# Performance work log

Hardware: AMD Instinct MI355X
Metric: run time of the kernel (lower is better)

Reference implementation:

```python
import jax, jax.numpy as jnp
import numpy as np
from jax import lax

VOCAB, EMB, H, L_CTX = 5, 64, 256, 100
HG = 2 * H  # generator hidden = 512


def lstm_cell(x, h, c, Wih, Whh, b):
    # PyTorch gate order: i, f, g, o
    z = x @ Wih.T + h @ Whh.T + b
    i, f, g, o = jnp.split(z, 4, axis=-1)
    c = jax.nn.sigmoid(f) * c + jax.nn.sigmoid(i) * jnp.tanh(g)
    h = jax.nn.sigmoid(o) * jnp.tanh(c)
    return h, c


def run_lstm(xs, Wih, Whh, b, hidden):
    # xs: [T, B, D] -> ys: [T, B, hidden]
    B = xs.shape[1]
    h0 = jnp.zeros((B, hidden), xs.dtype)

    def step(carry, x):
        h, c = carry
        h, c = lstm_cell(x, h, c, Wih, Whh, b)
        return (h, c), h

    _, ys = lax.scan(step, (h0, h0), xs)
    return ys


def bidir_layer(xs, Wih, Whh, b):
    # Wih/Whh/b stacked over directions: [2, ...]
    yf = run_lstm(xs, Wih[0], Whh[0], b[0], H)
    yb = run_lstm(xs[::-1], Wih[1], Whh[1], b[1], H)[::-1]
    return jnp.concatenate([yf, yb], axis=-1)  # [T, B, 2H]


def setup_inputs() -> dict:
    key = jax.random.key(0)
    ks = iter(jax.random.split(key, 24))
    s = 1.0 / np.sqrt(H)  # pytorch-style uniform scale -> use normal*s

    def w(shape):
        return (jax.random.normal(next(ks), shape, jnp.float32) * s).astype(jnp.float32)

    B = 1024
    inp = {
        "left_context": jax.random.randint(next(ks), (B, L_CTX), 0, VOCAB),
        "right_context": jax.random.randint(next(ks), (B, L_CTX), 0, VOCAB),
        "target_length": 256,
        "emb": w((VOCAB, EMB)),
        # bidirectional context LSTM, layer 0 (in=64) and layer 1 (in=512)
        "ctx0_Wih": w((2, 4 * H, EMB)),
        "ctx0_Whh": w((2, 4 * H, H)),
        "ctx0_b": w((2, 4 * H)),
        "ctx1_Wih": w((2, 4 * H, 2 * H)),
        "ctx1_Whh": w((2, 4 * H, H)),
        "ctx1_b": w((2, 4 * H)),
        # generator LSTM (hidden=512), layer 0 (in=64) and layer 1 (in=512)
        "gen0_Wih": w((4 * HG, EMB)),
        "gen0_Whh": w((4 * HG, HG)),
        "gen0_b": w((4 * HG,)),
        "gen1_Wih": w((4 * HG, HG)),
        "gen1_Whh": w((4 * HG, HG)),
        "gen1_b": w((4 * HG,)),
        "out_W": w((VOCAB, HG)),
        "out_b": w((VOCAB,)),
    }
    return inp


def reference(left_context, right_context, target_length, emb,
              ctx0_Wih, ctx0_Whh, ctx0_b, ctx1_Wih, ctx1_Whh, ctx1_b,
              gen0_Wih, gen0_Whh, gen0_b, gen1_Wih, gen1_Whh, gen1_b,
              out_W, out_b):
    B = left_context.shape[0]

    def encode(tokens):
        x = emb[tokens].transpose(1, 0, 2)          # [L, B, 64]
        x = bidir_layer(x, ctx0_Wih, ctx0_Whh, ctx0_b)  # dropout: eval -> identity
        x = bidir_layer(x, ctx1_Wih, ctx1_Whh, ctx1_b)
        return x                                     # [L, B, 512]

    left_final = encode(left_context)[-1]            # [B, 512]
    right_final = encode(right_context)[0]           # [B, 512]
    combined = (left_final + right_final) * 0.5

    # h_0 = combined repeated over both generator layers; c_0 = 0
    zeros = jnp.zeros((B, HG), combined.dtype)
    tok0 = jnp.zeros((B,), jnp.int32)

    def dec_step(carry, _):
        h0, c0, h1, c1, tok = carry
        x = emb[tok]                                 # [B, 64]
        h0, c0 = lstm_cell(x, h0, c0, gen0_Wih, gen0_Whh, gen0_b)
        h1, c1 = lstm_cell(h0, h1, c1, gen1_Wih, gen1_Whh, gen1_b)
        logits = h1 @ out_W.T + out_b                # dropout: eval -> identity
        tok = jnp.argmax(logits, axis=-1)
        return (h0, c0, h1, c1, tok), logits

    _, logits = lax.scan(dec_step, (combined, zeros, combined, zeros, tok0),
                         None, length=target_length)
    return logits.transpose(1, 0, 2)                 # [B, T, vocab]
```

## Files before the change

### kernel.cpp

```cpp
#include <hip/hip_runtime.h>


#define L_SEQ 100
#define BATCH 1024
#define HCTX 256
#define HG 512
#define TDEC 256

typedef __attribute__((ext_vector_type(8))) short bf16x8;
typedef __attribute__((ext_vector_type(4))) float f32x4;

__device__ __forceinline__ float sigf(float x){ return 1.0f/(1.0f+expf(-x)); }
__device__ __forceinline__ unsigned short f2bf(float x){
  unsigned int u = __float_as_uint(x);
  return (unsigned short)((u + 0x7fffu + ((u>>16)&1u)) >> 16);
}
__device__ __forceinline__ float bf2f(unsigned short h){
  return __uint_as_float(((unsigned int)h)<<16);
}

__global__ void pack_w(const float* __restrict__ W, int G, int K, int KTtot, int kt0,
                       unsigned short* __restrict__ hi, unsigned short* __restrict__ lo){
  int idx = blockIdx.x*blockDim.x + threadIdx.x;
  int kt_n = K/32;
  int total = (G/16)*kt_n*64;
  if (idx >= total) return;
  int lane = idx & 63;
  int ktl = (idx>>6) % kt_n;
  int gt  = (idx>>6) / kt_n;
  int g = gt*16 + (lane & 15);
  int k = ktl*32 + (lane>>4)*8;
  const float* src = W + (size_t)g*K + k;
  size_t dst = (((size_t)gt*KTtot + (kt0 + ktl))*64 + lane)*8;
  #pragma unroll
  for (int j=0;j<8;j++){
    float x = src[j];
    unsigned short h = f2bf(x);
    hi[dst+j] = h;
    lo[dst+j] = f2bf(x - bf2f(h));
  }
}

__global__ void embprep(const float* __restrict__ emb,
                        const float* __restrict__ c0Wih, const float* __restrict__ c0b,
                        const float* __restrict__ g0Wih, const float* __restrict__ g0b,
                        float* __restrict__ ectx0, float* __restrict__ egen0){
  int idx = blockIdx.x*blockDim.x + threadIdx.x;
  if (idx < 2*5*1024){
    int d = idx / 5120;
    int v = (idx / 1024) % 5;
    int j = idx % 1024;
    const float* w = c0Wih + ((size_t)d*1024 + j)*64;
    const float* e = emb + v*64;
    float s = c0b[d*1024 + j];
    #pragma unroll
    for (int k=0;k<64;k++) s += e[k]*w[k];
    ectx0[idx] = s;
  } else if (idx < 2*5*1024 + 5*2048){
    int i2 = idx - 10240;
    int v = i2 / 2048;
    int j = i2 % 2048;
    const float* w = g0Wih + (size_t)j*64;
    const float* e = emb + v*64;
    float s = g0b[j];
    #pragma unroll
    for (int k=0;k<64;k++) s += e[k]*w[k];
    egen0[i2] = s;
  }
}

__global__ void __launch_bounds__(512,1) ctx_l0_mfma(
    const int* __restrict__ toks,
    const float* __restrict__ ectx0,
    const unsigned short* __restrict__ wh, const unsigned short* __restrict__ wl,
    unsigned short* __restrict__ y0h, unsigned short* __restrict__ y0l)
{
  const int id  = blockIdx.x;
  const int dir = (id >> 2) & 1;
  const int bx  = ((id >> 3) << 2) | (id & 3);
  const int e0  = bx * 16;
  const int lane = threadIdx.x & 63;
  const int w    = threadIdx.x >> 6;
  const int lo16 = lane & 15, kgrp = lane >> 4;

  __shared__ unsigned short hsh[16*256];
  __shared__ unsigned short hsl[16*256];
  __shared__ float cs[16*256];
  for (int i=threadIdx.x;i<16*256;i+=512){ hsh[i]=0; hsl[i]=0; cs[i]=0.f; }
  __syncthreads();

  const unsigned short* pbh[4][2];
  const unsigned short* pbl[4][2];
  #pragma unroll
  for (int g=0;g<4;g++){
    #pragma unroll
    for (int st=0;st<2;st++){
      int ct = g*16 + w*2 + st;
      size_t off = (size_t)dir*1024*256 + ((size_t)(ct*8)*64 + lane)*8;
      pbh[g][st] = wh + off; pbl[g][st] = wl + off;
    }
  }
  const unsigned aoff0 = (unsigned)(lo16*512 + kgrp*16);
  const unsigned axor  = ((unsigned)(lo16 & 7)) << 4;

  for (int s=0;s<L_SEQ;s++){
    const int t = dir ? (L_SEQ-1-s) : s;
    f32x4 zero = {0.f,0.f,0.f,0.f};
    f32x4 acc[4][2];
    #pragma unroll
    for (int g=0;g<4;g++){
      #pragma unroll
      for (int st=0;st<2;st++) acc[g][st] = zero;
    }
    #pragma unroll 2
    for (int kt=0;kt<8;kt++){
      unsigned ao = (aoff0 + kt*64) ^ axor;
      bf16x8 ah = *(const bf16x8*)((const char*)hsh + ao);
      bf16x8 al = *(const bf16x8*)((const char*)hsl + ao);
      #pragma unroll
      for (int g=0;g<4;g++){
        #pragma unroll
        for (int st=0;st<2;st++){
          bf16x8 bh = *(const bf16x8*)(pbh[g][st] + (size_t)kt*512);
          bf16x8 bl = *(const bf16x8*)(pbl[g][st] + (size_t)kt*512);
          acc[g][st] = __builtin_amdgcn_mfma_f32_16x16x32_bf16(ah,bh,acc[g][st],0,0,0);
          acc[g][st] = __builtin_amdgcn_mfma_f32_16x16x32_bf16(al,bh,acc[g][st],0,0,0);
          acc[g][st] = __builtin_amdgcn_mfma_f32_16x16x32_bf16(ah,bl,acc[g][st],0,0,0);
        }
      }
    }
    __syncthreads();
    int tkr[4];
    #pragma unroll
    for (int r=0;r<4;r++) tkr[r] = toks[(e0 + kgrp*4 + r)*L_SEQ + t];
    #pragma unroll
    for (int st=0;st<2;st++){
      const int unit = w*32 + st*16 + lo16;
      #pragma unroll
      for (int r=0;r<4;r++){
        const int row = kgrp*4 + r;
        const int e = e0 + row;
        const float* ep = ectx0 + ((size_t)(dir*5 + tkr[r]))*1024 + unit;
        float zi = acc[0][st][r] + ep[0];
        float zf = acc[1][st][r] + ep[256];
        float zg = acc[2][st][r] + ep[512];
        float zo = acc[3][st][r] + ep[768];
        int ci = row*256 + unit;
        float c = sigf(zf)*cs[ci] + sigf(zi)*tanhf(zg);
        float h = sigf(zo)*tanhf(c);
        cs[ci] = c;
        unsigned short hb = f2bf(h), lb = f2bf(h - bf2f(hb));
        unsigned hoff = ((unsigned)(row*512 + unit*2)) ^ (((unsigned)(row & 7)) << 4);
        *(unsigned short*)((char*)hsh + hoff) = hb;
        *(unsigned short*)((char*)hsl + hoff) = lb;
        size_t yo = ((size_t)t*BATCH + e)*512 + dir*256 + unit;
        y0h[yo] = hb; y0l[yo] = lb;
      }
    }
    __syncthreads();
  }
}

__global__ void __launch_bounds__(512,1) ctx_l1_mfma(
    const unsigned short* __restrict__ y0h, const unsigned short* __restrict__ y0l,
    const unsigned short* __restrict__ wh, const unsigned short* __restrict__ wl,
    const float* __restrict__ bias,
    float* __restrict__ finals, int t_store)
{
  const int id  = blockIdx.x;
  const int dir = (id >> 2) & 1;
  const int bx  = ((id >> 3) << 2) | (id & 3);
  const int e0  = bx * 16;
  const int lane = threadIdx.x & 63;
  const int w    = threadIdx.x >> 6;
  const int lo16 = lane & 15, kgrp = lane >> 4;

  __shared__ unsigned short xsh[16*512];
  __shared__ unsigned short xsl[16*512];
  __shared__ unsigned short hsh[16*256];
  __shared__ unsigned short hsl[16*256];
  __shared__ float cs[16*256];
  for (int i=threadIdx.x;i<16*256;i+=512){ hsh[i]=0; hsl[i]=0; cs[i]=0.f; }

  float bb[4][2];
  #pragma unroll
  for (int g=0;g<4;g++){
    #pragma unroll
    for (int st=0;st<2;st++)
      bb[g][st] = bias[dir*1024 + g*256 + w*32 + st*16 + lo16];
  }
  const unsigned short* pbh[4][2];
  const unsigned short* pbl[4][2];
  #pragma unroll
  for (int g=0;g<4;g++){
    #pragma unroll
    for (int st=0;st<2;st++){
      int ct = g*16 + w*2 + st;
      size_t off = (size_t)dir*1024*768 + ((size_t)(ct*24)*64 + lane)*8;
      pbh[g][st] = wh + off; pbl[g][st] = wl + off;
    }
  }
  const unsigned axor = ((unsigned)(lo16 & 7)) << 4;
  __syncthreads();

  for (int s=0;s<L_SEQ;s++){
    const int t = dir ? (L_SEQ-1-s) : s;
    #pragma unroll
    for (int cc=0; cc<2; cc++){
      int ci = threadIdx.x + cc*512;
      int row = ci >> 6, cr = ci & 63;
      const unsigned short* srcbase = y0h + ((size_t)t*BATCH + e0 + row)*512 + cr*8;
      const unsigned short* srcbasel = y0l + ((size_t)t*BATCH + e0 + row)*512 + cr*8;
      uint4 vh = *(const uint4*)srcbase;
      uint4 vl = *(const uint4*)srcbasel;
      unsigned xo = ((unsigned)(row*1024 + cr*16)) ^ (((unsigned)(row & 7)) << 4);
      *(uint4*)((char*)xsh + xo) = vh;
      *(uint4*)((char*)xsl + xo) = vl;
    }
    __syncthreads();
    f32x4 zero = {0.f,0.f,0.f,0.f};
    f32x4 acc[4][2];
    #pragma unroll
    for (int g=0;g<4;g++){
      #pragma unroll
      for (int st=0;st<2;st++) acc[g][st] = zero;
    }
    #pragma unroll 2
    for (int kt=0;kt<16;kt++){
      unsigned ao = ((unsigned)(lo16*1024 + kt*64 + kgrp*16)) ^ axor;
      bf16x8 ah = *(const bf16x8*)((const char*)xsh + ao);
      bf16x8 al = *(const bf16x8*)((const char*)xsl + ao);
      #pragma unroll
      for (int g=0;g<4;g++){
        #pragma unroll
        for (int st=0;st<2;st++){
          bf16x8 bh = *(const bf16x8*)(pbh[g][st] + (size_t)kt*512);
          bf16x8 bl = *(const bf16x8*)(pbl[g][st] + (size_t)kt*512);
          acc[g][st] = __builtin_amdgcn_mfma_f32_16x16x32_bf16(ah,bh,acc[g][st],0,0,0);
          acc[g][st] = __builtin_amdgcn_mfma_f32_16x16x32_bf16(al,bh,acc[g][st],0,0,0);
          acc[g][st] = __builtin_amdgcn_mfma_f32_16x16x32_bf16(ah,bl,acc[g][st],0,0,0);
        }
      }
    }
    #pragma unroll 2
    for (int kt=16;kt<24;kt++){
      unsigned ao = ((unsigned)(lo16*512 + (kt-16)*64 + kgrp*16)) ^ axor;
      bf16x8 ah = *(const bf16x8*)((const char*)hsh + ao);
      bf16x8 al = *(const bf16x8*)((const char*)hsl + ao);
      #pragma unroll
      for (int g=0;g<4;g++){
        #pragma unroll
        for (int st=0;st<2;st++){
          bf16x8 bh = *(const bf16x8*)(pbh[g][st] + (size_t)kt*512);
          bf16x8 bl = *(const bf16x8*)(pbl[g][st] + (size_t)kt*512);
          acc[g][st] = __builtin_amdgcn_mfma_f32_16x16x32_bf16(ah,bh,acc[g][st],0,0,0);
          acc[g][st] = __builtin_amdgcn_mfma_f32_16x16x32_bf16(al,bh,acc[g][st],0,0,0);
          acc[g][st] = __builtin_amdgcn_mfma_f32_16x16x32_bf16(ah,bl,acc[g][st],0,0,0);
        }
      }
    }
    __syncthreads();
    #pragma unroll
    for (int st=0;st<2;st++){
      const int unit = w*32 + st*16 + lo16;
      #pragma unroll
      for (int r=0;r<4;r++){
        const int row = kgrp*4 + r;
        float zi = acc[0][st][r] + bb[0][st];
        float zf = acc[1][st][r] + bb[1][st];
        float zg = acc[2][st][r] + bb[2][st];
        float zo = acc[3][st][r] + bb[3][st];
        int ci = row*256 + unit;
        float c = sigf(zf)*cs[ci] + sigf(zi)*tanhf(zg);
        float h = sigf(zo)*tanhf(c);
        cs[ci] = c;
        unsigned short hb = f2bf(h), lb = f2bf(h - bf2f(hb));
        unsigned hoff = ((unsigned)(row*512 + unit*2)) ^ (((unsigned)(row & 7)) << 4);
        *(unsigned short*)((char*)hsh + hoff) = hb;
        *(unsigned short*)((char*)hsl + hoff) = lb;
        if (t == t_store)
          finals[(size_t)(e0 + row)*512 + dir*256 + unit] = h;
      }
    }
    __syncthreads();
  }
}

__global__ void combine_init2(const float* __restrict__ lf, const float* __restrict__ rf,
                              unsigned short* __restrict__ h0h, unsigned short* __restrict__ h0l,
                              unsigned short* __restrict__ h1h, unsigned short* __restrict__ h1l,
                              float* __restrict__ c0, float* __restrict__ c1,
                              int* __restrict__ tok){
  int i = blockIdx.x*blockDim.x + threadIdx.x;
  if (i < BATCH*HG){
    float v = 0.5f*(lf[i]+rf[i]);
    unsigned short h = f2bf(v);
    unsigned short l = f2bf(v - bf2f(h));
    h0h[i]=h; h0l[i]=l; h1h[i]=h; h1l[i]=l;
    c0[i]=0.f; c1[i]=0.f;
  }
  if (i < BATCH) tok[i]=0;
}

__global__ void __launch_bounds__(512,2) dec_l0_mfma(
    const int* __restrict__ tok,
    const float* __restrict__ egen0,
    const unsigned short* __restrict__ wh, const unsigned short* __restrict__ wl,
    const unsigned short* __restrict__ hih, const unsigned short* __restrict__ hil,
    unsigned short* __restrict__ hoh, unsigned short* __restrict__ hol,
    float* __restrict__ cst)
{
  const int bid = blockIdx.x;
  const int by = bid & 15;
  const int bx = bid >> 4;
  const int e0 = bx * 64;
  const int lane = threadIdx.x & 63;
  const int w = threadIdx.x >> 6;
  const int wm = w & 3;
  const int wu = w >> 2;
  const int ut = by*2 + wu;
  const int lo16 = lane & 15;
  const int kgrp = lane >> 4;
  const int row = e0 + wm*16 + lo16;

  const unsigned short* pah = hih + (size_t)row*512 + kgrp*8;
  const unsigned short* pal = hil + (size_t)row*512 + kgrp*8;
  const unsigned short* pb[8];
  #pragma unroll
  for (int q=0;q<4;q++){
    size_t off = ((size_t)(q*32+ut)*16*64 + lane)*8;
    pb[q]   = wh + off;
    pb[q+4] = wl + off;
  }
  f32x4 zero = {0.f,0.f,0.f,0.f};
  f32x4 acc[4] = {zero, zero, zero, zero};
  #pragma unroll 2
  for (int ks=0; ks<16; ks++){
    bf16x8 ah = *(const bf16x8*)(pah + ks*32);
    bf16x8 al = *(const bf16x8*)(pal + ks*32);
    #pragma unroll
    for (int q=0;q<4;q++){
      bf16x8 bh = *(const bf16x8*)(pb[q]   + ks*512);
      bf16x8 bl = *(const bf16x8*)(pb[q+4] + ks*512);
      acc[q] = __builtin_amdgcn_mfma_f32_16x16x32_bf16(ah, bh, acc[q], 0,0,0);
      acc[q] = __builtin_amdgcn_mfma_f32_16x16x32_bf16(al, bh, acc[q], 0,0,0);
      acc[q] = __builtin_amdgcn_mfma_f32_16x16x32_bf16(ah, bl, acc[q], 0,0,0);
    }
  }
  const int u = ut*16 + lo16;
  const int r0 = e0 + wm*16 + kgrp*4;
  #pragma unroll
  for (int r=0;r<4;r++){
    const int e = r0 + r;
    const int tk = tok[e];
    const float* ep = egen0 + (size_t)tk*2048 + u;
    float zi = acc[0][r] + ep[0];
    float zf = acc[1][r] + ep[512];
    float zg = acc[2][r] + ep[1024];
    float zo = acc[3][r] + ep[1536];
    const size_t idx = (size_t)e*512 + u;
    float c = sigf(zf)*cst[idx] + sigf(zi)*tanhf(zg);
    float h = sigf(zo)*tanhf(c);
    cst[idx] = c;
    unsigned short hb = f2bf(h);
    hoh[idx] = hb;
    hol[idx] = f2bf(h - bf2f(hb));
  }
}

__global__ void __launch_bounds__(512,2) dec_l1_mfma(
    const unsigned short* __restrict__ xh, const unsigned short* __restrict__ xl,
    const unsigned short* __restrict__ wh, const unsigned short* __restrict__ wl,
    const float* __restrict__ bias,
    const unsigned short* __restrict__ hih, const unsigned short* __restrict__ hil,
    unsigned short* __restrict__ hoh, unsigned short* __restrict__ hol,
    float* __restrict__ cst)
{
  const int bid = blockIdx.x;
  const int by = bid & 15;
  const int bx = bid >> 4;
  const int e0 = bx * 64;
  const int lane = threadIdx.x & 63;
  const int w = threadIdx.x >> 6;
  const int wm = w & 3;
  const int wu = w >> 2;
  const int ut = by*2 + wu;
  const int lo16 = lane & 15;
  const int kgrp = lane >> 4;
  const int row = e0 + wm*16 + lo16;

  const unsigned short* pxh = xh  + (size_t)row*512 + kgrp*8;
  const unsigned short* pxl = xl  + (size_t)row*512 + kgrp*8;
  const unsigned short* pah = hih + (size_t)row*512 + kgrp*8;
  const unsigned short* pal = hil + (size_t)row*512 + kgrp*8;
  const unsigned short* pb[8];
  #pragma unroll
  for (int q=0;q<4;q++){
    size_t off = ((size_t)(q*32+ut)*32*64 + lane)*8;
    pb[q]   = wh + off;
    pb[q+4] = wl + off;
  }
  f32x4 zero = {0.f,0.f,0.f,0.f};
  f32x4 acc[4] = {zero, zero, zero, zero};
  #pragma unroll 2
  for (int ks=0; ks<16; ks++){
    bf16x8 ah = *(const bf16x8*)(pxh + ks*32);
    bf16x8 al = *(const bf16x8*)(pxl + ks*32);
    #pragma unroll
    for (int q=0;q<4;q++){
      bf16x8 bh = *(const bf16x8*)(pb[q]   + ks*512);
      bf16x8 bl = *(const bf16x8*)(pb[q+4] + ks*512);
      acc[q] = __builtin_amdgcn_mfma_f32_16x16x32_bf16(ah, bh, acc[q], 0,0,0);
      acc[q] = __builtin_amdgcn_mfma_f32_16x16x32_bf16(al, bh, acc[q], 0,0,0);
      acc[q] = __builtin_amdgcn_mfma_f32_16x16x32_bf16(ah, bl, acc[q], 0,0,0);
    }
  }
  #pragma unroll 2
  for (int ks=16; ks<32; ks++){
    bf16x8 ah = *(const bf16x8*)(pah + (ks-16)*32);
    bf16x8 al = *(const bf16x8*)(pal + (ks-16)*32);
    #pragma unroll
    for (int q=0;q<4;q++){
      bf16x8 bh = *(const bf16x8*)(pb[q]   + ks*512);
      bf16x8 bl = *(const bf16x8*)(pb[q+4] + ks*512);
      acc[q] = __builtin_amdgcn_mfma_f32_16x16x32_bf16(ah, bh, acc[q], 0,0,0);
      acc[q] = __builtin_amdgcn_mfma_f32_16x16x32_bf16(al, bh, acc[q], 0,0,0);
      acc[q] = __builtin_amdgcn_mfma_f32_16x16x32_bf16(ah, bl, acc[q], 0,0,0);
    }
  }
  const int u = ut*16 + lo16;
  const int r0 = e0 + wm*16 + kgrp*4;
  const float b0 = bias[u], b1 = bias[512+u], b2 = bias[1024+u], b3 = bias[1536+u];
  #pragma unroll
  for (int r=0;r<4;r++){
    const int e = r0 + r;
    float zi = acc[0][r] + b0;
    float zf = acc[1][r] + b1;
    float zg = acc[2][r] + b2;
    float zo = acc[3][r] + b3;
    const size_t idx = (size_t)e*512 + u;
    float c = sigf(zf)*cst[idx] + sigf(zi)*tanhf(zg);
    float h = sigf(zo)*tanhf(c);
    cst[idx] = c;
    unsigned short hb = f2bf(h);
    hoh[idx] = hb;
    hol[idx] = f2bf(h - bf2f(hb));
  }
}

__global__ void dec_out(const unsigned short* __restrict__ h1h,
                        const unsigned short* __restrict__ h1l,
                        const float* __restrict__ outW,
                        const float* __restrict__ outb,
                        float* __restrict__ out,
                        int* __restrict__ tok, int t){
  const int lane = threadIdx.x & 63;
  const int e = blockIdx.x*4 + (threadIdx.x >> 6);
  const unsigned short* hh = h1h + (size_t)e*512;
  const unsigned short* hl = h1l + (size_t)e*512;
  float s0=0,s1=0,s2=0,s3=0,s4=0;
  for (int k=lane;k<512;k+=64){
    float hv = bf2f(hh[k]) + bf2f(hl[k]);
    s0 += hv*outW[k];
    s1 += hv*outW[512+k];
    s2 += hv*outW[1024+k];
    s3 += hv*outW[1536+k];
    s4 += hv*outW[2048+k];
  }
  #pragma unroll
  for (int off=32; off>0; off>>=1){
    s0 += __shfl_down(s0, off);
    s1 += __shfl_down(s1, off);
    s2 += __shfl_down(s2, off);
    s3 += __shfl_down(s3, off);
    s4 += __shfl_down(s4, off);
  }
  if (lane==0){
    float l[5] = { s0+outb[0], s1+outb[1], s2+outb[2], s3+outb[3], s4+outb[4] };
    float* op = out + ((size_t)e*TDEC + t)*5;
    float best = l[0]; int bi = 0;
    op[0] = l[0];
    #pragma unroll
    for (int v=1;v<5;v++){
      op[v] = l[v];
      if (l[v] > best){ best = l[v]; bi = v; }
    }
    tok[e] = bi;
  }
}

extern "C" void kernel_launch(void* const* d_in, const int* in_sizes, int n_in,
                              void* d_out, int out_size, void* d_ws, size_t ws_size,
                              hipStream_t stream){
  (void)in_sizes; (void)n_in; (void)out_size;
  const int*   leftc    = (const int*)d_in[0];
  const int*   rightc   = (const int*)d_in[1];
  const float* emb      = (const float*)d_in[3];
  const float* ctx0_Wih = (const float*)d_in[4];
  const float* ctx0_Whh = (const float*)d_in[5];
  const float* ctx0_b   = (const float*)d_in[6];
  const float* ctx1_Wih = (const float*)d_in[7];
  const float* ctx1_Whh = (const float*)d_in[8];
  const float* ctx1_b   = (const float*)d_in[9];
  const float* gen0_Wih = (const float*)d_in[10];
  const float* gen0_Whh = (const float*)d_in[11];
  const float* gen0_b   = (const float*)d_in[12];
  const float* gen1_Wih = (const float*)d_in[13];
  const float* gen1_Whh = (const float*)d_in[14];
  const float* gen1_b   = (const float*)d_in[15];
  const float* out_W    = (const float*)d_in[16];
  const float* out_b    = (const float*)d_in[17];
  float* out = (float*)d_out;

  char* p = (char*)d_ws;
  auto carve = [&](size_t nfloats)->float*{
    float* r = (float*)p;
    p += ((nfloats*sizeof(float) + 255) & ~(size_t)255);
    return r;
  };
  auto carveu = [&](size_t nush)->unsigned short*{
    return (unsigned short*)carve((nush + 1)/2);
  };
  float* ectx0  = carve(2*5*1024);
  float* egen0  = carve(5*2048);
  float* leftF  = carve((size_t)BATCH*HG);
  float* rightF = carve((size_t)BATCH*HG);
  float* c0s    = carve((size_t)BATCH*HG);
  float* c1s    = carve((size_t)BATCH*HG);
  unsigned short* c0pkh = carveu((size_t)2*1024*256);
  unsigned short* c0pkl = carveu((size_t)2*1024*256);
  unsigned short* c1pkh = carveu((size_t)2*1024*768);
  unsigned short* c1pkl = carveu((size_t)2*1024*768);
  unsigned short* pk0h = carveu((size_t)2048*512);
  unsigned short* pk0l = carveu((size_t)2048*512);
  unsigned short* pk1h = carveu((size_t)2048*1024);
  unsigned short* pk1l = carveu((size_t)2048*1024);
  unsigned short* h0ha = carveu((size_t)BATCH*HG);
  unsigned short* h0la = carveu((size_t)BATCH*HG);
  unsigned short* h0hb = carveu((size_t)BATCH*HG);
  unsigned short* h0lb = carveu((size_t)BATCH*HG);
  unsigned short* h1ha = carveu((size_t)BATCH*HG);
  unsigned short* h1la = carveu((size_t)BATCH*HG);
  unsigned short* h1hb = carveu((size_t)BATCH*HG);
  unsigned short* h1lb = carveu((size_t)BATCH*HG);
  int*   tok    = (int*)carve(BATCH);
  unsigned short* y0h = carveu((size_t)L_SEQ*BATCH*512);
  unsigned short* y0l = carveu((size_t)L_SEQ*BATCH*512);
  if ((size_t)(p - (char*)d_ws) > ws_size) return;

  for (int d=0; d<2; d++){
    pack_w<<<128, 256, 0, stream>>>(ctx0_Whh + (size_t)d*1024*256, 1024, 256, 8, 0,
                                    c0pkh + (size_t)d*1024*256/ (size_t)1 * 0 + (size_t)d*262144,
                                    c0pkl + (size_t)d*262144);
    pack_w<<<256, 256, 0, stream>>>(ctx1_Wih + (size_t)d*1024*512, 1024, 512, 24, 0,
                                    c1pkh + (size_t)d*786432, c1pkl + (size_t)d*786432);
    pack_w<<<128, 256, 0, stream>>>(ctx1_Whh + (size_t)d*1024*256, 1024, 256, 24, 16,
                                    c1pkh + (size_t)d*786432, c1pkl + (size_t)d*786432);
  }
  pack_w<<<512, 256, 0, stream>>>(gen0_Whh, 2048, 512, 16,  0, pk0h, pk0l);
  pack_w<<<512, 256, 0, stream>>>(gen1_Wih, 2048, 512, 32,  0, pk1h, pk1l);
  pack_w<<<512, 256, 0, stream>>>(gen1_Whh, 2048, 512, 32, 16, pk1h, pk1l);

  embprep<<<(20480+255)/256, 256, 0, stream>>>(emb, ctx0_Wih, ctx0_b,
                                               gen0_Wih, gen0_b, ectx0, egen0);

  ctx_l0_mfma<<<128, 512, 0, stream>>>(leftc, ectx0, c0pkh, c0pkl, y0h, y0l);
  ctx_l1_mfma<<<128, 512, 0, stream>>>(y0h, y0l, c1pkh, c1pkl, ctx1_b, leftF, L_SEQ-1);
  ctx_l0_mfma<<<128, 512, 0, stream>>>(rightc, ectx0, c0pkh, c0pkl, y0h, y0l);
  ctx_l1_mfma<<<128, 512, 0, stream>>>(y0h, y0l, c1pkh, c1pkl, ctx1_b, rightF, 0);

  combine_init2<<<(BATCH*HG+255)/256, 256, 0, stream>>>(leftF, rightF,
                                                        h0ha, h0la, h1ha, h1la,
                                                        c0s, c1s, tok);

  for (int t=0;t<TDEC;t++){
    unsigned short* h0ih = (t&1)? h0hb : h0ha;
    unsigned short* h0il = (t&1)? h0lb : h0la;
    unsigned short* h0oh = (t&1)? h0ha : h0hb;
    unsigned short* h0ol = (t&1)? h0la : h0lb;
    unsigned short* h1ih = (t&1)? h1hb : h1ha;
    unsigned short* h1il = (t&1)? h1lb : h1la;
    unsigned short* h1oh = (t&1)? h1ha : h1hb;
    unsigned short* h1ol = (t&1)? h1la : h1lb;
    dec_l0_mfma<<<256, 512, 0, stream>>>(tok, egen0, pk0h, pk0l,
                                         h0ih, h0il, h0oh, h0ol, c0s);
    dec_l1_mfma<<<256, 512, 0, stream>>>(h0oh, h0ol, pk1h, pk1l, gen1_b,
                                         h1ih, h1il, h1oh, h1ol, c1s);
    dec_out<<<256, 256, 0, stream>>>(h1oh, h1ol, out_W, out_b, out, tok, t);
  }
}
```

Baseline: 23.13 ms.

## Fuse decoder timesteps into one persistent cooperative kernel with grid syncs

Replaces the 768 per-timestep launches of the two generator LSTM layers and the output projection with a single cooperative kernel that loops over time. Layers are separated by grid.sync, and the cell states stay in registers instead of global memory. The output projection is fused as a shuffle reduction plus atomicAdd into a bias-prefilled output, and the next token is recomputed from the previous logits. The MFMA accumulators are also split into three separate chains. The cost is two grid-wide barriers per step, a dependence on all 256 blocks being co-resident, and atomics whose summation order is not fixed.

```diff
diff --git a/kernel.cpp b/kernel.cpp
--- a/kernel.cpp
+++ b/kernel.cpp
@@ -1,4 +1,7 @@
 #include <hip/hip_runtime.h>
+#include <hip/hip_cooperative_groups.h>
+
+namespace cg = cooperative_groups;
 
 
 #define L_SEQ 100
@@ -69,6 +72,11 @@
   }
 }
 
+__global__ void prefill_out(float* __restrict__ out, const float* __restrict__ outb){
+  int i = blockIdx.x*blockDim.x + threadIdx.x;
+  if (i < BATCH*TDEC*5) out[i] = outb[i%5];
+}
+
 __global__ void __launch_bounds__(512,1) ctx_l0_mfma(
     const int* __restrict__ toks,
     const float* __restrict__ ectx0,
@@ -288,28 +296,29 @@
 
 __global__ void combine_init2(const float* __restrict__ lf, const float* __restrict__ rf,
                               unsigned short* __restrict__ h0h, unsigned short* __restrict__ h0l,
-                              unsigned short* __restrict__ h1h, unsigned short* __restrict__ h1l,
-                              float* __restrict__ c0, float* __restrict__ c1,
-                              int* __restrict__ tok){
+                              unsigned short* __restrict__ h1h, unsigned short* __restrict__ h1l){
   int i = blockIdx.x*blockDim.x + threadIdx.x;
   if (i < BATCH*HG){
     float v = 0.5f*(lf[i]+rf[i]);
     unsigned short h = f2bf(v);
     unsigned short l = f2bf(v - bf2f(h));
     h0h[i]=h; h0l[i]=l; h1h[i]=h; h1l[i]=l;
-    c0[i]=0.f; c1[i]=0.f;
-  }
-  if (i < BATCH) tok[i]=0;
-}
-
-__global__ void __launch_bounds__(512,2) dec_l0_mfma(
-    const int* __restrict__ tok,
+  }
+}
+
+__global__ void __launch_bounds__(512,2) dec_persist(
     const float* __restrict__ egen0,
-    const unsigned short* __restrict__ wh, const unsigned short* __restrict__ wl,
-    const unsigned short* __restrict__ hih, const unsigned short* __restrict__ hil,
-    unsigned short* __restrict__ hoh, unsigned short* __restrict__ hol,
-    float* __restrict__ cst)
+    const unsigned short* __restrict__ w0h, const unsigned short* __restrict__ w0l,
+    const unsigned short* __restrict__ w1h, const unsigned short* __restrict__ w1l,
+    const float* __restrict__ bias1,
+    const float* __restrict__ outW,
+    unsigned short* __restrict__ h0ha, unsigned short* __restrict__ h0la,
+    unsigned short* __restrict__ h0hb, unsigned short* __restrict__ h0lb,
+    unsigned short* __restrict__ h1ha, unsigned short* __restrict__ h1la,
+    unsigned short* __restrict__ h1hb, unsigned short* __restrict__ h1lb,
+    float* __restrict__ out)
 {
+  cg::grid_group grid = cg::this_grid();
   const int bid = blockIdx.x;
   const int by = bid & 15;
   const int bx = bid >> 4;
@@ -321,171 +330,154 @@
   const int ut = by*2 + wu;
   const int lo16 = lane & 15;
   const int kgrp = lane >> 4;
-  const int row = e0 + wm*16 + lo16;
-
-  const unsigned short* pah = hih + (size_t)row*512 + kgrp*8;
-  const unsigned short* pal = hil + (size_t)row*512 + kgrp*8;
-  const unsigned short* pb[8];
+  const int arow = e0 + wm*16 + lo16;
+  const int u = ut*16 + lo16;
+  const int r0 = e0 + wm*16 + kgrp*4;
+
+  const float b10 = bias1[u], b11 = bias1[512+u];
+  const float b12 = bias1[1024+u], b13 = bias1[1536+u];
+  float ow[5];
+  #pragma unroll
+  for (int v=0;v<5;v++) ow[v] = outW[v*512 + u];
+
+  const unsigned short* p0[8];
+  const unsigned short* p1[8];
   #pragma unroll
   for (int q=0;q<4;q++){
-    size_t off = ((size_t)(q*32+ut)*16*64 + lane)*8;
-    pb[q]   = wh + off;
-    pb[q+4] = wl + off;
-  }
-  f32x4 zero = {0.f,0.f,0.f,0.f};
-  f32x4 acc[4] = {zero, zero, zero, zero};
-  #pragma unroll 2
-  for (int ks=0; ks<16; ks++){
-    bf16x8 ah = *(const bf16x8*)(pah + ks*32);
-    bf16x8 al = *(const bf16x8*)(pal + ks*32);
-    #pragma unroll
-    for (int q=0;q<4;q++){
-      bf16x8 bh = *(const bf16x8*)(pb[q]   + ks*512);
-      bf16x8 bl = *(const bf16x8*)(pb[q+4] + ks*512);
-      acc[q] = __builtin_amdgcn_mfma_f32_16x16x32_bf16(ah, bh, acc[q], 0,0,0);
-      acc[q] = __builtin_amdgcn_mfma_f32_16x16x32_bf16(al, bh, acc[q], 0,0,0);
-      acc[q] = __builtin_amdgcn_mfma_f32_16x16x32_bf16(ah, bl, acc[q], 0,0,0);
-    }
-  }
-  const int u = ut*16 + lo16;
-  const int r0 = e0 + wm*16 + kgrp*4;
-  #pragma unroll
-  for (int r=0;r<4;r++){
-    const int e = r0 + r;
-    const int tk = tok[e];
-    const float* ep = egen0 + (size_t)tk*2048 + u;
-    float zi = acc[0][r] + ep[0];
-    float zf = acc[1][r] + ep[512];
-    float zg = acc[2][r] + ep[1024];
-    float zo = acc[3][r] + ep[1536];
-    const size_t idx = (size_t)e*512 + u;
-    float c = sigf(zf)*cst[idx] + sigf(zi)*tanhf(zg);
-    float h = sigf(zo)*tanhf(c);
-    cst[idx] = c;
-    unsigned short hb = f2bf(h);
-    hoh[idx] = hb;
-    hol[idx] = f2bf(h - bf2f(hb));
-  }
-}
-
-__global__ void __launch_bounds__(512,2) dec_l1_mfma(
-    const unsigned short* __restrict__ xh, const unsigned short* __restrict__ xl,
-    const unsigned short* __restrict__ wh, const unsigned short* __restrict__ wl,
-    const float* __restrict__ bias,
-    const unsigned short* __restrict__ hih, const unsigned short* __restrict__ hil,
-    unsigned short* __restrict__ hoh, unsigned short* __restrict__ hol,
-    float* __restrict__ cst)
-{
-  const int bid = blockIdx.x;
-  const int by = bid & 15;
-  const int bx = bid >> 4;
-  const int e0 = bx * 64;
-  const int lane = threadIdx.x & 63;
-  const int w = threadIdx.x >> 6;
-  const int wm = w & 3;
-  const int wu = w >> 2;
-  const int ut = by*2 + wu;
-  const int lo16 = lane & 15;
-  const int kgrp = lane >> 4;
-  const int row = e0 + wm*16 + lo16;
-
-  const unsigned short* pxh = xh  + (size_t)row*512 + kgrp*8;
-  const unsigned short* pxl = xl  + (size_t)row*512 + kgrp*8;
-  const unsigned short* pah = hih + (size_t)row*512 + kgrp*8;
-  const unsigned short* pal = hil + (size_t)row*512 + kgrp*8;
-  const unsigned short* pb[8];
-  #pragma unroll
-  for (int q=0;q<4;q++){
-    size_t off = ((size_t)(q*32+ut)*32*64 + lane)*8;
-    pb[q]   = wh + off;
-    pb[q+4] = wl + off;
-  }
-  f32x4 zero = {0.f,0.f,0.f,0.f};
-  f32x4 acc[4] = {zero, zero, zero, zero};
-  #pragma unroll 2
-  for (int ks=0; ks<16; ks++){
-    bf16x8 ah = *(const bf16x8*)(pxh + ks*32);
-    bf16x8 al = *(const bf16x8*)(pxl + ks*32);
-    #pragma unroll
-    for (int q=0;q<4;q++){
-      bf16x8 bh = *(const bf16x8*)(pb[q]   + ks*512);
-      bf16x8 bl = *(const bf16x8*)(pb[q+4] + ks*512);
-      acc[q] = __builtin_amdgcn_mfma_f32_16x16x32_bf16(ah, bh, acc[q], 0,0,0);
-      acc[q] = __builtin_amdgcn_mfma_f32_16x16x32_bf16(al, bh, acc[q], 0,0,0);
-      acc[q] = __builtin_amdgcn_mfma_f32_16x16x32_bf16(ah, bl, acc[q], 0,0,0);
-    }
-  }
-  #pragma unroll 2
-  for (int ks=16; ks<32; ks++){
-    bf16x8 ah = *(const bf16x8*)(pah + (ks-16)*32);
-    bf16x8 al = *(const bf16x8*)(pal + (ks-16)*32);
-    #pragma unroll
-    for (int q=0;q<4;q++){
-      bf16x8 bh = *(const bf16x8*)(pb[q]   + ks*512);
-      bf16x8 bl = *(const bf16x8*)(pb[q+4] + ks*512);
-      acc[q] = __builtin_amdgcn_mfma_f32_16x16x32_bf16(ah, bh, acc[q], 0,0,0);
-      acc[q] = __builtin_amdgcn_mfma_f32_16x16x32_bf16(al, bh, acc[q], 0,0,0);
-      acc[q] = __builtin_amdgcn_mfma_f32_16x16x32_bf16(ah, bl, acc[q], 0,0,0);
-    }
-  }
-  const int u = ut*16 + lo16;
-  const int r0 = e0 + wm*16 + kgrp*4;
-  const float b0 = bias[u], b1 = bias[512+u], b2 = bias[1024+u], b3 = bias[1536+u];
-  #pragma unroll
-  for (int r=0;r<4;r++){
-    const int e = r0 + r;
-    float zi = acc[0][r] + b0;
-    float zf = acc[1][r] + b1;
-    float zg = acc[2][r] + b2;
-    float zo = acc[3][r] + b3;
-    const size_t idx = (size_t)e*512 + u;
-    float c = sigf(zf)*cst[idx] + sigf(zi)*tanhf(zg);
-    float h = sigf(zo)*tanhf(c);
-    cst[idx] = c;
-    unsigned short hb = f2bf(h);
-    hoh[idx] = hb;
-    hol[idx] = f2bf(h - bf2f(hb));
-  }
-}
-
-__global__ void dec_out(const unsigned short* __restrict__ h1h,
-                        const unsigned short* __restrict__ h1l,
-                        const float* __restrict__ outW,
-                        const float* __restrict__ outb,
-                        float* __restrict__ out,
-                        int* __restrict__ tok, int t){
-  const int lane = threadIdx.x & 63;
-  const int e = blockIdx.x*4 + (threadIdx.x >> 6);
-  const unsigned short* hh = h1h + (size_t)e*512;
-  const unsigned short* hl = h1l + (size_t)e*512;
-  float s0=0,s1=0,s2=0,s3=0,s4=0;
-  for (int k=lane;k<512;k+=64){
-    float hv = bf2f(hh[k]) + bf2f(hl[k]);
-    s0 += hv*outW[k];
-    s1 += hv*outW[512+k];
-    s2 += hv*outW[1024+k];
-    s3 += hv*outW[1536+k];
-    s4 += hv*outW[2048+k];
-  }
-  #pragma unroll
-  for (int off=32; off>0; off>>=1){
-    s0 += __shfl_down(s0, off);
-    s1 += __shfl_down(s1, off);
-    s2 += __shfl_down(s2, off);
-    s3 += __shfl_down(s3, off);
-    s4 += __shfl_down(s4, off);
-  }
-  if (lane==0){
-    float l[5] = { s0+outb[0], s1+outb[1], s2+outb[2], s3+outb[3], s4+outb[4] };
-    float* op = out + ((size_t)e*TDEC + t)*5;
-    float best = l[0]; int bi = 0;
-    op[0] = l[0];
-    #pragma unroll
-    for (int v=1;v<5;v++){
-      op[v] = l[v];
-      if (l[v] > best){ best = l[v]; bi = v; }
-    }
-    tok[e] = bi;
+    size_t o0 = ((size_t)(q*32+ut)*16*64 + lane)*8;
+    p0[q] = w0h + o0; p0[q+4] = w0l + o0;
+    size_t o1 = ((size_t)(q*32+ut)*32*64 + lane)*8;
+    p1[q] = w1h + o1; p1[q+4] = w1l + o1;
+  }
+  float c0r[4] = {0.f,0.f,0.f,0.f};
+  float c1r[4] = {0.f,0.f,0.f,0.f};
+  const f32x4 z4 = {0.f,0.f,0.f,0.f};
+
+  for (int t=0;t<TDEC;t++){
+    const unsigned short* h0ih = (t&1)? h0hb : h0ha;
+    const unsigned short* h0il = (t&1)? h0lb : h0la;
+    unsigned short* h0oh = (t&1)? h0ha : h0hb;
+    unsigned short* h0ol = (t&1)? h0la : h0lb;
+    const unsigned short* h1ih = (t&1)? h1hb : h1ha;
+    const unsigned short* h1il = (t&1)? h1lb : h1la;
+    unsigned short* h1oh = (t&1)? h1ha : h1hb;
+    unsigned short* h1ol = (t&1)? h1la : h1lb;
+
+    {
+      const unsigned short* pah = h0ih + (size_t)arow*512 + kgrp*8;
+      const unsigned short* pal = h0il + (size_t)arow*512 + kgrp*8;
+      f32x4 aHH[4]={z4,z4,z4,z4}, aLH[4]={z4,z4,z4,z4}, aHL[4]={z4,z4,z4,z4};
+      #pragma unroll 2
+      for (int ks=0;ks<16;ks++){
+        bf16x8 ah = *(const bf16x8*)(pah + ks*32);
+        bf16x8 al = *(const bf16x8*)(pal + ks*32);
+        #pragma unroll
+        for (int q=0;q<4;q++){
+          bf16x8 bh = *(const bf16x8*)(p0[q]   + (size_t)ks*512);
+          bf16x8 bl = *(const bf16x8*)(p0[q+4] + (size_t)ks*512);
+          aHH[q] = __builtin_amdgcn_mfma_f32_16x16x32_bf16(ah,bh,aHH[q],0,0,0);
+          aLH[q] = __builtin_amdgcn_mfma_f32_16x16x32_bf16(al,bh,aLH[q],0,0,0);
+          aHL[q] = __builtin_amdgcn_mfma_f32_16x16x32_bf16(ah,bl,aHL[q],0,0,0);
+        }
+      }
+      int tkr[4];
+      #pragma unroll
+      for (int r=0;r<4;r++){
+        int tk = 0;
+        if (t > 0){
+          const float* lp = out + ((size_t)(r0+r)*TDEC + (t-1))*5;
+          float l0=lp[0],l1=lp[1],l2=lp[2],l3=lp[3],l4=lp[4];
+          float best=l0;
+          if (l1>best){best=l1;tk=1;}
+          if (l2>best){best=l2;tk=2;}
+          if (l3>best){best=l3;tk=3;}
+          if (l4>best){best=l4;tk=4;}
+        }
+        tkr[r]=tk;
+      }
+      #pragma unroll
+      for (int r=0;r<4;r++){
+        const int e = r0 + r;
+        const float* ep = egen0 + (size_t)tkr[r]*2048 + u;
+        float zi = aHH[0][r]+aLH[0][r]+aHL[0][r] + ep[0];
+        float zf = aHH[1][r]+aLH[1][r]+aHL[1][r] + ep[512];
+        float zg = aHH[2][r]+aLH[2][r]+aHL[2][r] + ep[1024];
+        float zo = aHH[3][r]+aLH[3][r]+aHL[3][r] + ep[1536];
+        float c = sigf(zf)*c0r[r] + sigf(zi)*tanhf(zg);
+        float h = sigf(zo)*tanhf(c);
+        c0r[r] = c;
+        const size_t idx = (size_t)e*512 + u;
+        unsigned short hb = f2bf(h);
+        h0oh[idx] = hb;
+        h0ol[idx] = f2bf(h - bf2f(hb));
+      }
+    }
+    grid.sync();
+
+    {
+      const unsigned short* pxh = h0oh + (size_t)arow*512 + kgrp*8;
+      const unsigned short* pxl = h0ol + (size_t)arow*512 + kgrp*8;
+      const unsigned short* pah = h1ih + (size_t)arow*512 + kgrp*8;
+      const unsigned short* pal = h1il + (size_t)arow*512 + kgrp*8;
+      f32x4 aHH[4]={z4,z4,z4,z4}, aLH[4]={z4,z4,z4,z4}, aHL[4]={z4,z4,z4,z4};
+      #pragma unroll 2
+      for (int ks=0;ks<16;ks++){
+        bf16x8 ah = *(const bf16x8*)(pxh + ks*32);
+        bf16x8 al = *(const bf16x8*)(pxl + ks*32);
+        #pragma unroll
+        for (int q=0;q<4;q++){
+          bf16x8 bh = *(const bf16x8*)(p1[q]   + (size_t)ks*512);
+          bf16x8 bl = *(const bf16x8*)(p1[q+4] + (size_t)ks*512);
+          aHH[q] = __builtin_amdgcn_mfma_f32_16x16x32_bf16(ah,bh,aHH[q],0,0,0);
+          aLH[q] = __builtin_amdgcn_mfma_f32_16x16x32_bf16(al,bh,aLH[q],0,0,0);
+          aHL[q] = __builtin_amdgcn_mfma_f32_16x16x32_bf16(ah,bl,aHL[q],0,0,0);
+        }
+      }
+      #pragma unroll 2
+      for (int ks=16;ks<32;ks++){
+        bf16x8 ah = *(const bf16x8*)(pah + (ks-16)*32);
+        bf16x8 al = *(const bf16x8*)(pal + (ks-16)*32);
+        #pragma unroll
+        for (int q=0;q<4;q++){
+          bf16x8 bh = *(const bf16x8*)(p1[q]   + (size_t)ks*512);
+          bf16x8 bl = *(const bf16x8*)(p1[q+4] + (size_t)ks*512);
+          aHH[q] = __builtin_amdgcn_mfma_f32_16x16x32_bf16(ah,bh,aHH[q],0,0,0);
+          aLH[q] = __builtin_amdgcn_mfma_f32_16x16x32_bf16(al,bh,aLH[q],0,0,0);
+          aHL[q] = __builtin_amdgcn_mfma_f32_16x16x32_bf16(ah,bl,aHL[q],0,0,0);
+        }
+      }
+      float hv[4];
+      #pragma unroll
+      for (int r=0;r<4;r++){
+        const int e = r0 + r;
+        float zi = aHH[0][r]+aLH[0][r]+aHL[0][r] + b10;
+        float zf = aHH[1][r]+aLH[1][r]+aHL[1][r] + b11;
+        float zg = aHH[2][r]+aLH[2][r]+aHL[2][r] + b12;
+        float zo = aHH[3][r]+aLH[3][r]+aHL[3][r] + b13;
+        float c = sigf(zf)*c1r[r] + sigf(zi)*tanhf(zg);
+        float h = sigf(zo)*tanhf(c);
+        c1r[r] = c;
+        hv[r] = h;
+        const size_t idx = (size_t)e*512 + u;
+        unsigned short hb = f2bf(h);
+        h1oh[idx] = hb;
+        h1ol[idx] = f2bf(h - bf2f(hb));
+      }
+      #pragma unroll
+      for (int r=0;r<4;r++){
+        #pragma unroll
+        for (int v=0;v<5;v++){
+          float psum = hv[r]*ow[v];
+          psum += __shfl_xor(psum, 1);
+          psum += __shfl_xor(psum, 2);
+          psum += __shfl_xor(psum, 4);
+          psum += __shfl_xor(psum, 8);
+          if (lo16 == 0)
+            atomicAdd(out + ((size_t)(r0+r)*TDEC + t)*5 + v, psum);
+        }
+      }
+    }
+    grid.sync();
   }
 }
 
@@ -525,8 +517,6 @@
   float* egen0  = carve(5*2048);
   float* leftF  = carve((size_t)BATCH*HG);
   float* rightF = carve((size_t)BATCH*HG);
-  float* c0s    = carve((size_t)BATCH*HG);
-  float* c1s    = carve((size_t)BATCH*HG);
   unsigned short* c0pkh = carveu((size_t)2*1024*256);
   unsigned short* c0pkl = carveu((size_t)2*1024*256);
   unsigned short* c1pkh = carveu((size_t)2*1024*768);
@@ -543,15 +533,13 @@
   unsigned short* h1la = carveu((size_t)BATCH*HG);
   unsigned short* h1hb = carveu((size_t)BATCH*HG);
   unsigned short* h1lb = carveu((size_t)BATCH*HG);
-  int*   tok    = (int*)carve(BATCH);
   unsigned short* y0h = carveu((size_t)L_SEQ*BATCH*512);
   unsigned short* y0l = carveu((size_t)L_SEQ*BATCH*512);
   if ((size_t)(p - (char*)d_ws) > ws_size) return;
 
   for (int d=0; d<2; d++){
     pack_w<<<128, 256, 0, stream>>>(ctx0_Whh + (size_t)d*1024*256, 1024, 256, 8, 0,
-                                    c0pkh + (size_t)d*1024*256/ (size_t)1 * 0 + (size_t)d*262144,
-                                    c0pkl + (size_t)d*262144);
+                                    c0pkh + (size_t)d*262144, c0pkl + (size_t)d*262144);
     pack_w<<<256, 256, 0, stream>>>(ctx1_Wih + (size_t)d*1024*512, 1024, 512, 24, 0,
                                     c1pkh + (size_t)d*786432, c1pkl + (size_t)d*786432);
     pack_w<<<128, 256, 0, stream>>>(ctx1_Whh + (size_t)d*1024*256, 1024, 256, 24, 16,
@@ -563,6 +551,7 @@
 
   embprep<<<(20480+255)/256, 256, 0, stream>>>(emb, ctx0_Wih, ctx0_b,
                                                gen0_Wih, gen0_b, ectx0, egen0);
+  prefill_out<<<(BATCH*TDEC*5+255)/256, 256, 0, stream>>>(out, out_b);
 
   ctx_l0_mfma<<<128, 512, 0, stream>>>(leftc, ectx0, c0pkh, c0pkl, y0h, y0l);
   ctx_l1_mfma<<<128, 512, 0, stream>>>(y0h, y0l, c1pkh, c1pkl, ctx1_b, leftF, L_SEQ-1);
@@ -570,22 +559,15 @@
   ctx_l1_mfma<<<128, 512, 0, stream>>>(y0h, y0l, c1pkh, c1pkl, ctx1_b, rightF, 0);
 
   combine_init2<<<(BATCH*HG+255)/256, 256, 0, stream>>>(leftF, rightF,
-                                                        h0ha, h0la, h1ha, h1la,
-                                                        c0s, c1s, tok);
-
-  for (int t=0;t<TDEC;t++){
-    unsigned short* h0ih = (t&1)? h0hb : h0ha;
-    unsigned short* h0il = (t&1)? h0lb : h0la;
-    unsigned short* h0oh = (t&1)? h0ha : h0hb;
-    unsigned short* h0ol = (t&1)? h0la : h0lb;
-    unsigned short* h1ih = (t&1)? h1hb : h1ha;
-    unsigned short* h1il = (t&1)? h1lb : h1la;
-    unsigned short* h1oh = (t&1)? h1ha : h1hb;
-    unsigned short* h1ol = (t&1)? h1la : h1lb;
-    dec_l0_mfma<<<256, 512, 0, stream>>>(tok, egen0, pk0h, pk0l,
-                                         h0ih, h0il, h0oh, h0ol, c0s);
-    dec_l1_mfma<<<256, 512, 0, stream>>>(h0oh, h0ol, pk1h, pk1l, gen1_b,
-                                         h1ih, h1il, h1oh, h1ol, c1s);
-    dec_out<<<256, 256, 0, stream>>>(h1oh, h1ol, out_W, out_b, out, tok, t);
-  }
-}
+                                                        h0ha, h0la, h1ha, h1la);
+
+  void* kargs[] = {
+    (void*)&egen0, (void*)&pk0h, (void*)&pk0l, (void*)&pk1h, (void*)&pk1l,
+    (void*)&gen1_b, (void*)&out_W,
+    (void*)&h0ha, (void*)&h0la, (void*)&h0hb, (void*)&h0lb,
+    (void*)&h1ha, (void*)&h1la, (void*)&h1hb, (void*)&h1lb,
+    (void*)&out
+  };
+  hipLaunchCooperativeKernel((void*)dec_persist, dim3(256), dim3(512),
+                             kargs, 0, stream);
+}
```

New measurement: 45.66 ms. 97.4% more time.
